# Kernel optimization log

Measured on AMD Instinct MI355X. Metric: run time of the kernel, lower is better.

## Reference

```python
import jax, jax.numpy as jnp
import numpy as np

N_NODES = 200000
N_EDGES = 6400000
IN_CH = 256
HID = 16


def gcn_conv(h, src, dst, deg_inv_sqrt, W, b, n_nodes):
    """One GCNConv (PyG semantics: add self-loops, symmetric norm, linear, scatter-add, bias)."""
    hw = h @ W  # [N, out]
    norm = deg_inv_sqrt[src] * deg_inv_sqrt[dst]  # [E]
    agg = jax.ops.segment_sum(norm[:, None] * hw[src], dst, num_segments=n_nodes)
    # self-loop contribution: deg_inv_sqrt[i]^2 * hw[i]
    agg = agg + hw * (deg_inv_sqrt ** 2)[:, None]
    return agg + b


def setup_inputs() -> dict:
    key = jax.random.key(0)
    k_x, k_e, k_w1, k_w2, k_w3 = jax.random.split(key, 5)
    x = jax.random.normal(k_x, (N_NODES, IN_CH), dtype=jnp.float32)
    edge_index = jax.random.randint(k_e, (2, N_EDGES), 0, N_NODES, dtype=jnp.int64)
    # Glorot-ish init for the three GCNConv weights, zeros for biases (PyG default)
    W1 = jax.random.normal(k_w1, (IN_CH, HID), dtype=jnp.float32) * (1.0 / np.sqrt(IN_CH))
    b1 = jnp.zeros((HID,), dtype=jnp.float32)
    W2 = jax.random.normal(k_w2, (HID, HID), dtype=jnp.float32) * (1.0 / np.sqrt(HID))
    b2 = jnp.zeros((HID,), dtype=jnp.float32)
    W3 = jax.random.normal(k_w3, (HID, 1), dtype=jnp.float32) * (1.0 / np.sqrt(HID))
    b3 = jnp.zeros((1,), dtype=jnp.float32)
    return {"x": x, "edge_index": edge_index, "W1": W1, "b1": b1,
            "W2": W2, "b2": b2, "W3": W3, "b3": b3}


def reference(x, edge_index, W1, b1, W2, b2, W3, b3):
    n_nodes = x.shape[0]
    src, dst = edge_index[0], edge_index[1]
    # GCN norm with self-loops: deg counts incoming edges + 1 self-loop
    deg = jax.ops.segment_sum(jnp.ones_like(dst, dtype=x.dtype), dst,
                              num_segments=n_nodes) + 1.0
    deg_inv_sqrt = deg ** -0.5  # deg >= 1, safe
    h = jax.nn.relu(gcn_conv(x, src, dst, deg_inv_sqrt, W1, b1, n_nodes))
    # dropout is identity in eval mode
    h = jax.nn.relu(gcn_conv(h, src, dst, deg_inv_sqrt, W2, b2, n_nodes))
    out = gcn_conv(h, src, dst, deg_inv_sqrt, W3, b3, n_nodes)  # [N, 1]
    return out
```

## Files before the change

kernel.cpp:

```cpp
#include <hip/hip_runtime.h>

#define NN 200000
#define EE 6400000L
#define NCB 196
#define CAP 36864
#define TILE 8192
#define NTILE 782

__device__ inline void f4add(float4& a, const float4 v) {
    a.x += v.x; a.y += v.y; a.z += v.z; a.w += v.w;
}

__global__ void k_detect(const int* __restrict__ w, int* __restrict__ flag,
                         int* __restrict__ gcur) {
    __shared__ int any;
    if (threadIdx.x == 0) any = 0;
    __syncthreads();
    int found = 0;
    for (int i = threadIdx.x; i < 8192; i += 256)
        if (w[2 * i + 1] != 0) found = 1;
    if (found) atomicOr(&any, 1);
    if (threadIdx.x < NCB) gcur[threadIdx.x] = threadIdx.x * CAP;
    __syncthreads();
    if (threadIdx.x == 0) flag[0] = any ? 0 : 1;
}

__global__ __launch_bounds__(256) void k_passA(
    const int* __restrict__ ew, const int* __restrict__ flag,
    int* __restrict__ gcur, unsigned* __restrict__ stage, long e) {
    __shared__ unsigned lv[TILE];
    __shared__ unsigned char lb[TILE];
    __shared__ int lh[NCB], lseg[NCB], lcur[NCB];
    for (int i = threadIdx.x; i < NCB; i += 256) { lh[i] = 0; lcur[i] = 0; }
    __syncthreads();
    long t0 = (long)blockIdx.x * TILE;
    int cnt = (int)min((long)TILE, e - t0);
    int shift = *flag;
    for (int i = threadIdx.x; i < cnt; i += 256) {
        int s = ew[(t0 + i) << shift];
        int d = ew[(EE + t0 + i) << shift];
        int b = d >> 10;
        lv[i] = (unsigned)s | ((unsigned)(d & 1023) << 18);
        lb[i] = (unsigned char)b;
        atomicAdd(&lh[b], 1);
    }
    __syncthreads();
    for (int i = threadIdx.x; i < NCB; i += 256)
        if (lh[i]) lseg[i] = atomicAdd(&gcur[i], lh[i]);
    __syncthreads();
    for (int i = threadIdx.x; i < cnt; i += 256) {
        int b = lb[i];
        int r = atomicAdd(&lcur[b], 1);
        stage[lseg[b] + r] = lv[i];
    }
}

__global__ __launch_bounds__(1024) void k_sortB(
    const unsigned* __restrict__ stage, const int* __restrict__ gcur,
    float* __restrict__ dis, int* __restrict__ offn, int* __restrict__ degn,
    unsigned* __restrict__ csr, int n) {
    __shared__ int cnt[1024];
    __shared__ int cur[1024];
    __shared__ int wsum[16];
    int t = threadIdx.x, B = blockIdx.x;
    cnt[t] = 0;
    __syncthreads();
    int s0 = B * CAP, s1 = gcur[B];
    for (int i = s0 + t; i < s1; i += 1024)
        atomicAdd(&cnt[stage[i] >> 18], 1);
    __syncthreads();
    int c = cnt[t];
    int lane = t & 63, w = t >> 6;
    int s = c;
#pragma unroll
    for (int o = 1; o < 64; o <<= 1) {
        int u = __shfl_up(s, o, 64);
        if (lane >= o) s += u;
    }
    if (lane == 63) wsum[w] = s;
    __syncthreads();
    int add = 0;
    for (int k = 0; k < w; ++k) add += wsum[k];
    int excl = s - c + add;
    cur[t] = excl;
    int node = B * 1024 + t;
    if (node < n) {
        offn[node] = s0 + excl;
        degn[node] = c;
        dis[node] = rsqrtf((float)(c + 1));
    }
    __syncthreads();
    for (int i = s0 + t; i < s1; i += 1024) {
        unsigned v = stage[i];
        int pos = s0 + atomicAdd(&cur[v >> 18], 1);
        csr[pos] = v & 0x3FFFF;
    }
}

__global__ __launch_bounds__(256) void k_mm1(
    const float* __restrict__ x, const float* __restrict__ W,
    const float* __restrict__ dis, float* __restrict__ hws, int n) {
    __shared__ float Wl[256 * 16];
    int t = threadIdx.x;
#pragma unroll
    for (int i = 0; i < 4; ++i)
        ((float4*)Wl)[t + i * 256] = ((const float4*)W)[t + i * 256];
    __syncthreads();

    int node = blockIdx.x * 256 + t;
    if (node >= n) return;

    const float4* xr = (const float4*)(x + (long)node * 256);
    float acc[16];
#pragma unroll
    for (int o = 0; o < 16; ++o) acc[o] = 0.f;

#pragma unroll 8
    for (int kk = 0; kk < 64; ++kk) {
        float4 xv = xr[kk];
#pragma unroll
        for (int q = 0; q < 4; ++q) {
            float xs = (q == 0) ? xv.x : (q == 1) ? xv.y : (q == 2) ? xv.z : xv.w;
            const float4* wr = (const float4*)&Wl[(kk * 4 + q) * 16];
#pragma unroll
            for (int oo = 0; oo < 4; ++oo) {
                float4 wv = wr[oo];
                acc[oo * 4 + 0] = fmaf(xs, wv.x, acc[oo * 4 + 0]);
                acc[oo * 4 + 1] = fmaf(xs, wv.y, acc[oo * 4 + 1]);
                acc[oo * 4 + 2] = fmaf(xs, wv.z, acc[oo * 4 + 2]);
                acc[oo * 4 + 3] = fmaf(xs, wv.w, acc[oo * 4 + 3]);
            }
        }
    }
    float dv = dis[node];
    float4* hwo = (float4*)(hws + (long)node * 16);
#pragma unroll
    for (int oo = 0; oo < 4; ++oo)
        hwo[oo] = make_float4(acc[oo * 4] * dv, acc[oo * 4 + 1] * dv,
                              acc[oo * 4 + 2] * dv, acc[oo * 4 + 3] * dv);
}

__global__ __launch_bounds__(256) void k_mm2(
    const float* __restrict__ h, const float* __restrict__ W,
    const float* __restrict__ dis, float* __restrict__ hws, int n) {
    __shared__ float Wl[256];
    if (threadIdx.x < 64) ((float4*)Wl)[threadIdx.x] = ((const float4*)W)[threadIdx.x];
    __syncthreads();
    int node = blockIdx.x * 256 + threadIdx.x;
    if (node >= n) return;
    float hv[16];
    const float4* hr = (const float4*)(h + (long)node * 16);
#pragma unroll
    for (int i = 0; i < 4; ++i) {
        float4 v = hr[i];
        hv[i * 4 + 0] = v.x; hv[i * 4 + 1] = v.y; hv[i * 4 + 2] = v.z; hv[i * 4 + 3] = v.w;
    }
    float acc[16];
#pragma unroll
    for (int o = 0; o < 16; ++o) acc[o] = 0.f;
#pragma unroll
    for (int k = 0; k < 16; ++k) {
        float xs = hv[k];
#pragma unroll
        for (int o = 0; o < 16; ++o) acc[o] = fmaf(xs, Wl[k * 16 + o], acc[o]);
    }
    float dv = dis[node];
    float4* hwo = (float4*)(hws + (long)node * 16);
#pragma unroll
    for (int oo = 0; oo < 4; ++oo)
        hwo[oo] = make_float4(acc[oo * 4] * dv, acc[oo * 4 + 1] * dv,
                              acc[oo * 4 + 2] * dv, acc[oo * 4 + 3] * dv);
}

__global__ __launch_bounds__(256) void k_mm3(
    const float* __restrict__ h, const float* __restrict__ W,
    const float* __restrict__ dis, float* __restrict__ hws3, int n) {
    int node = blockIdx.x * 256 + threadIdx.x;
    if (node >= n) return;
    const float4* hr = (const float4*)(h + (long)node * 16);
    float acc = 0.f;
#pragma unroll
    for (int i = 0; i < 4; ++i) {
        float4 v = hr[i];
        acc = fmaf(v.x, W[i * 4 + 0], acc);
        acc = fmaf(v.y, W[i * 4 + 1], acc);
        acc = fmaf(v.z, W[i * 4 + 2], acc);
        acc = fmaf(v.w, W[i * 4 + 3], acc);
    }
    hws3[node] = acc * dis[node];
}

template <int RELU>
__global__ __launch_bounds__(256) void k_g16(
    const int* __restrict__ offn, const int* __restrict__ degn,
    const unsigned* __restrict__ csr, const float* __restrict__ dis,
    const float* __restrict__ hws, const float* __restrict__ b,
    float* __restrict__ h, int n) {
    int t = threadIdx.x;
    int node = blockIdx.x * 64 + (t >> 2);
    int q = t & 3;
    if (node >= n) return;
    int s0 = offn[node];
    int dg = degn[node];
    const float4* tab = (const float4*)hws;
    float4 a0 = make_float4(0.f, 0.f, 0.f, 0.f);
    float4 a1 = make_float4(0.f, 0.f, 0.f, 0.f);
    float4 a2 = make_float4(0.f, 0.f, 0.f, 0.f);
    float4 a3 = make_float4(0.f, 0.f, 0.f, 0.f);
    int k = 0;
    for (; k + 3 < dg; k += 4) {
        unsigned e0 = csr[s0 + k], e1 = csr[s0 + k + 1];
        unsigned e2 = csr[s0 + k + 2], e3 = csr[s0 + k + 3];
        f4add(a0, tab[(long)e0 * 4 + q]);
        f4add(a1, tab[(long)e1 * 4 + q]);
        f4add(a2, tab[(long)e2 * 4 + q]);
        f4add(a3, tab[(long)e3 * 4 + q]);
    }
    for (; k < dg; ++k)
        f4add(a0, tab[(long)csr[s0 + k] * 4 + q]);
    f4add(a0, a1); f4add(a2, a3); f4add(a0, a2);
    f4add(a0, tab[(long)node * 4 + q]);
    float dv = dis[node];
    float4 bb = ((const float4*)b)[q];
    float4 r = make_float4(fmaf(dv, a0.x, bb.x), fmaf(dv, a0.y, bb.y),
                           fmaf(dv, a0.z, bb.z), fmaf(dv, a0.w, bb.w));
    if (RELU) {
        r.x = fmaxf(r.x, 0.f); r.y = fmaxf(r.y, 0.f);
        r.z = fmaxf(r.z, 0.f); r.w = fmaxf(r.w, 0.f);
    }
    ((float4*)(h + (long)node * 16))[q] = r;
}

__global__ __launch_bounds__(256) void k_g1(
    const int* __restrict__ offn, const int* __restrict__ degn,
    const unsigned* __restrict__ csr, const float* __restrict__ dis,
    const float* __restrict__ hws3, const float* __restrict__ b,
    float* __restrict__ out, int n) {
    int t = threadIdx.x;
    int node = blockIdx.x * 16 + (t >> 4);
    int ln = t & 15;
    if (node >= n) return;
    int s0 = offn[node], dg = degn[node];
    float acc = 0.f;
    for (int k = ln; k < dg; k += 16)
        acc += hws3[csr[s0 + k]];
#pragma unroll
    for (int o = 8; o >= 1; o >>= 1) acc += __shfl_down(acc, o, 16);
    if (ln == 0)
        out[node] = fmaf(dis[node], acc + hws3[node], b[0]);
}

extern "C" void kernel_launch(void* const* d_in, const int* in_sizes, int n_in,
                              void* d_out, int out_size, void* d_ws, size_t ws_size,
                              hipStream_t stream) {
    const float* x  = (const float*)d_in[0];
    const int*   ew = (const int*)d_in[1];
    const float* W1 = (const float*)d_in[2];
    const float* b1 = (const float*)d_in[3];
    const float* W2 = (const float*)d_in[4];
    const float* b2 = (const float*)d_in[5];
    const float* W3 = (const float*)d_in[6];
    const float* b3 = (const float*)d_in[7];
    float* out = (float*)d_out;

    unsigned* stage = (unsigned*)d_ws;
    unsigned* csr   = stage + (long)NCB * CAP;
    int*      gcur  = (int*)(csr + (long)NCB * CAP);
    int*      flag  = gcur + 256;
    int*      offn  = flag + 16;
    int*      degn  = offn + 200704;
    float*    dis   = (float*)(degn + 200704);
    float*    bufA  = dis + 200704;
    float*    bufB  = bufA + 3276800;

    const int n = NN;
    const long e = EE;
    int nb = (n + 255) / 256;
    int gb = (n + 63) / 64;
    int g1b = (n + 15) / 16;

    k_detect<<<1, 256, 0, stream>>>(ew, flag, gcur);
    k_passA<<<NTILE, 256, 0, stream>>>(ew, flag, gcur, stage, e);
    k_sortB<<<NCB, 1024, 0, stream>>>(stage, gcur, dis, offn, degn, csr, n);

    k_mm1<<<nb, 256, 0, stream>>>(x, W1, dis, bufA, n);
    k_g16<1><<<gb, 256, 0, stream>>>(offn, degn, csr, dis, bufA, b1, bufB, n);
    k_mm2<<<nb, 256, 0, stream>>>(bufB, W2, dis, bufA, n);
    k_g16<1><<<gb, 256, 0, stream>>>(offn, degn, csr, dis, bufA, b2, bufB, n);
    k_mm3<<<nb, 256, 0, stream>>>(bufB, W3, dis, bufA, n);
    k_g1<<<g1b, 256, 0, stream>>>(offn, degn, csr, dis, bufA, b3, out, n);
}
```

Measured before the change: 473.4 us.

## Split hidden features into four float4 planes and gather per plane

Node feature buffers move from row-major [N,16] to four planar float4 arrays, one per 4-channel quarter. The gather kernel now runs one quarter per block range, with 16 lanes per node striding over that node's edges and a shuffle reduction at the end. Each quarter table is 3.2 MB instead of 12.8 MB, so the random gathers should hit cache more often. The cost is that every edge index is read four times and each block does a cross-lane reduction.

```diff
diff --git a/kernel.cpp b/kernel.cpp
--- a/kernel.cpp
+++ b/kernel.cpp
@@ -6,6 +6,8 @@
 #define CAP 36864
 #define TILE 8192
 #define NTILE 782
+#define QSTRIDE 200064
+#define GB16 12500
 
 __device__ inline void f4add(float4& a, const float4 v) {
     a.x += v.x; a.y += v.y; a.z += v.z; a.w += v.w;
@@ -99,7 +101,7 @@
 
 __global__ __launch_bounds__(256) void k_mm1(
     const float* __restrict__ x, const float* __restrict__ W,
-    const float* __restrict__ dis, float* __restrict__ hws, int n) {
+    const float* __restrict__ dis, float4* __restrict__ outq, int n) {
     __shared__ float Wl[256 * 16];
     int t = threadIdx.x;
 #pragma unroll
@@ -133,26 +135,24 @@
         }
     }
     float dv = dis[node];
-    float4* hwo = (float4*)(hws + (long)node * 16);
-#pragma unroll
-    for (int oo = 0; oo < 4; ++oo)
-        hwo[oo] = make_float4(acc[oo * 4] * dv, acc[oo * 4 + 1] * dv,
-                              acc[oo * 4 + 2] * dv, acc[oo * 4 + 3] * dv);
+#pragma unroll
+    for (int q = 0; q < 4; ++q)
+        outq[q * QSTRIDE + node] = make_float4(acc[q * 4] * dv, acc[q * 4 + 1] * dv,
+                                               acc[q * 4 + 2] * dv, acc[q * 4 + 3] * dv);
 }
 
 __global__ __launch_bounds__(256) void k_mm2(
-    const float* __restrict__ h, const float* __restrict__ W,
-    const float* __restrict__ dis, float* __restrict__ hws, int n) {
+    const float4* __restrict__ hq, const float* __restrict__ W,
+    const float* __restrict__ dis, float4* __restrict__ outq, int n) {
     __shared__ float Wl[256];
     if (threadIdx.x < 64) ((float4*)Wl)[threadIdx.x] = ((const float4*)W)[threadIdx.x];
     __syncthreads();
     int node = blockIdx.x * 256 + threadIdx.x;
     if (node >= n) return;
     float hv[16];
-    const float4* hr = (const float4*)(h + (long)node * 16);
 #pragma unroll
     for (int i = 0; i < 4; ++i) {
-        float4 v = hr[i];
+        float4 v = hq[i * QSTRIDE + node];
         hv[i * 4 + 0] = v.x; hv[i * 4 + 1] = v.y; hv[i * 4 + 2] = v.z; hv[i * 4 + 3] = v.w;
     }
     float acc[16];
@@ -165,23 +165,21 @@
         for (int o = 0; o < 16; ++o) acc[o] = fmaf(xs, Wl[k * 16 + o], acc[o]);
     }
     float dv = dis[node];
-    float4* hwo = (float4*)(hws + (long)node * 16);
-#pragma unroll
-    for (int oo = 0; oo < 4; ++oo)
-        hwo[oo] = make_float4(acc[oo * 4] * dv, acc[oo * 4 + 1] * dv,
-                              acc[oo * 4 + 2] * dv, acc[oo * 4 + 3] * dv);
+#pragma unroll
+    for (int q = 0; q < 4; ++q)
+        outq[q * QSTRIDE + node] = make_float4(acc[q * 4] * dv, acc[q * 4 + 1] * dv,
+                                               acc[q * 4 + 2] * dv, acc[q * 4 + 3] * dv);
 }
 
 __global__ __launch_bounds__(256) void k_mm3(
-    const float* __restrict__ h, const float* __restrict__ W,
+    const float4* __restrict__ hq, const float* __restrict__ W,
     const float* __restrict__ dis, float* __restrict__ hws3, int n) {
     int node = blockIdx.x * 256 + threadIdx.x;
     if (node >= n) return;
-    const float4* hr = (const float4*)(h + (long)node * 16);
     float acc = 0.f;
 #pragma unroll
     for (int i = 0; i < 4; ++i) {
-        float4 v = hr[i];
+        float4 v = hq[i * QSTRIDE + node];
         acc = fmaf(v.x, W[i * 4 + 0], acc);
         acc = fmaf(v.y, W[i * 4 + 1], acc);
         acc = fmaf(v.z, W[i * 4 + 2], acc);
@@ -191,44 +189,48 @@
 }
 
 template <int RELU>
-__global__ __launch_bounds__(256) void k_g16(
+__global__ __launch_bounds__(256) void k_g16p(
     const int* __restrict__ offn, const int* __restrict__ degn,
     const unsigned* __restrict__ csr, const float* __restrict__ dis,
-    const float* __restrict__ hws, const float* __restrict__ b,
-    float* __restrict__ h, int n) {
+    const float4* __restrict__ tabq, const float* __restrict__ b,
+    float4* __restrict__ outq, int n) {
+    int bid = blockIdx.x;
+    int q = bid / GB16;
+    int g = bid - q * GB16;
     int t = threadIdx.x;
-    int node = blockIdx.x * 64 + (t >> 2);
-    int q = t & 3;
-    if (node >= n) return;
-    int s0 = offn[node];
-    int dg = degn[node];
-    const float4* tab = (const float4*)hws;
+    int node = g * 16 + (t >> 4);
+    int ln = t & 15;
+    if (node >= n) return;
+    const float4* tab = tabq + (long)q * QSTRIDE;
+    int s0 = offn[node], dg = degn[node];
     float4 a0 = make_float4(0.f, 0.f, 0.f, 0.f);
     float4 a1 = make_float4(0.f, 0.f, 0.f, 0.f);
-    float4 a2 = make_float4(0.f, 0.f, 0.f, 0.f);
-    float4 a3 = make_float4(0.f, 0.f, 0.f, 0.f);
-    int k = 0;
-    for (; k + 3 < dg; k += 4) {
-        unsigned e0 = csr[s0 + k], e1 = csr[s0 + k + 1];
-        unsigned e2 = csr[s0 + k + 2], e3 = csr[s0 + k + 3];
-        f4add(a0, tab[(long)e0 * 4 + q]);
-        f4add(a1, tab[(long)e1 * 4 + q]);
-        f4add(a2, tab[(long)e2 * 4 + q]);
-        f4add(a3, tab[(long)e3 * 4 + q]);
-    }
-    for (; k < dg; ++k)
-        f4add(a0, tab[(long)csr[s0 + k] * 4 + q]);
-    f4add(a0, a1); f4add(a2, a3); f4add(a0, a2);
-    f4add(a0, tab[(long)node * 4 + q]);
-    float dv = dis[node];
-    float4 bb = ((const float4*)b)[q];
-    float4 r = make_float4(fmaf(dv, a0.x, bb.x), fmaf(dv, a0.y, bb.y),
-                           fmaf(dv, a0.z, bb.z), fmaf(dv, a0.w, bb.w));
-    if (RELU) {
-        r.x = fmaxf(r.x, 0.f); r.y = fmaxf(r.y, 0.f);
-        r.z = fmaxf(r.z, 0.f); r.w = fmaxf(r.w, 0.f);
-    }
-    ((float4*)(h + (long)node * 16))[q] = r;
+    int k = ln;
+    for (; k + 16 < dg; k += 32) {
+        f4add(a0, tab[csr[s0 + k]]);
+        f4add(a1, tab[csr[s0 + k + 16]]);
+    }
+    if (k < dg) f4add(a0, tab[csr[s0 + k]]);
+    f4add(a0, a1);
+#pragma unroll
+    for (int o = 8; o >= 1; o >>= 1) {
+        a0.x += __shfl_xor(a0.x, o, 16);
+        a0.y += __shfl_xor(a0.y, o, 16);
+        a0.z += __shfl_xor(a0.z, o, 16);
+        a0.w += __shfl_xor(a0.w, o, 16);
+    }
+    if (ln == 0) {
+        f4add(a0, tab[node]);
+        float dv = dis[node];
+        float4 bb = ((const float4*)b)[q];
+        float4 r = make_float4(fmaf(dv, a0.x, bb.x), fmaf(dv, a0.y, bb.y),
+                               fmaf(dv, a0.z, bb.z), fmaf(dv, a0.w, bb.w));
+        if (RELU) {
+            r.x = fmaxf(r.x, 0.f); r.y = fmaxf(r.y, 0.f);
+            r.z = fmaxf(r.z, 0.f); r.w = fmaxf(r.w, 0.f);
+        }
+        outq[(long)q * QSTRIDE + node] = r;
+    }
 }
 
 __global__ __launch_bounds__(256) void k_g1(
@@ -270,13 +272,12 @@
     int*      offn  = flag + 16;
     int*      degn  = offn + 200704;
     float*    dis   = (float*)(degn + 200704);
-    float*    bufA  = dis + 200704;
-    float*    bufB  = bufA + 3276800;
+    float4*   bufA  = (float4*)(dis + 200704);
+    float4*   bufB  = bufA + 4 * QSTRIDE;
 
     const int n = NN;
     const long e = EE;
     int nb = (n + 255) / 256;
-    int gb = (n + 63) / 64;
     int g1b = (n + 15) / 16;
 
     k_detect<<<1, 256, 0, stream>>>(ew, flag, gcur);
@@ -284,9 +285,9 @@
     k_sortB<<<NCB, 1024, 0, stream>>>(stage, gcur, dis, offn, degn, csr, n);
 
     k_mm1<<<nb, 256, 0, stream>>>(x, W1, dis, bufA, n);
-    k_g16<1><<<gb, 256, 0, stream>>>(offn, degn, csr, dis, bufA, b1, bufB, n);
+    k_g16p<1><<<4 * GB16, 256, 0, stream>>>(offn, degn, csr, dis, bufA, b1, bufB, n);
     k_mm2<<<nb, 256, 0, stream>>>(bufB, W2, dis, bufA, n);
-    k_g16<1><<<gb, 256, 0, stream>>>(offn, degn, csr, dis, bufA, b2, bufB, n);
-    k_mm3<<<nb, 256, 0, stream>>>(bufB, W3, dis, bufA, n);
-    k_g1<<<g1b, 256, 0, stream>>>(offn, degn, csr, dis, bufA, b3, out, n);
-}
+    k_g16p<1><<<4 * GB16, 256, 0, stream>>>(offn, degn, csr, dis, bufA, b2, bufB, n);
+    k_mm3<<<nb, 256, 0, stream>>>(bufB, W3, dis, (float*)bufA, n);
+    k_g1<<<g1b, 256, 0, stream>>>(offn, degn, csr, dis, (const float*)bufA, b3, out, n);
+}
```

After: 499.7 us. +5.6%, slower.
